# Kernel tuning notes

Measured on AMD Instinct MI355X. Metric: run time of the kernel, lower is better.

The kernel has to match this reference:

```python
import jax, jax.numpy as jnp
import numpy as np

DIM = 512
NUM_EXPERTS = 8
HID = 4 * DIM
B, S = 2, 2048


def setup_inputs() -> dict:
    key = jax.random.key(0)
    ks = jax.random.split(key, 7)
    sc = 0.02
    x = jax.random.normal(ks[0], (B, S, DIM), dtype=jnp.float32)
    Wr = jax.random.normal(ks[1], (DIM, NUM_EXPERTS), dtype=jnp.float32) * sc
    br = jnp.zeros((NUM_EXPERTS,), dtype=jnp.float32)
    W1 = jax.random.normal(ks[2], (NUM_EXPERTS, DIM, HID), dtype=jnp.float32) * sc
    b1 = jnp.zeros((NUM_EXPERTS, HID), dtype=jnp.float32)
    W2 = jax.random.normal(ks[3], (NUM_EXPERTS, HID, DIM), dtype=jnp.float32) * sc
    b2 = jnp.zeros((NUM_EXPERTS, DIM), dtype=jnp.float32)
    return {"x": x, "Wr": Wr, "br": br, "W1": W1, "b1": b1, "W2": W2, "b2": b2}


def reference(x, Wr, br, W1, b1, W2, b2):
    b, s, d = x.shape
    E = Wr.shape[1]
    xf = x.reshape(-1, d)                                   # [N, d]
    N = xf.shape[0]
    logits = xf @ Wr + br                                   # [N, E]
    probs = jax.nn.softmax(logits, axis=-1)
    top_w, top_idx = jax.lax.top_k(probs, 2)                # [N, 2]
    top_w = jax.nn.softmax(top_w, axis=-1)                  # renormalize top-2
    # combine weight per (token, expert); topk indices are distinct so add is safe
    comb = jnp.zeros((N, E), dtype=xf.dtype)
    comb = comb.at[jnp.arange(N)[:, None], top_idx].add(top_w)  # [N, E]
    # dense per-expert MLP (eval mode: dropout is identity); exact GELU as nn.GELU
    h = jax.nn.gelu(jnp.einsum('nd,edf->enf', xf, W1) + b1[:, None, :], approximate=False)
    y = jnp.einsum('enf,efd->end', h, W2) + b2[:, None, :]  # [E, N, d]
    out = jnp.einsum('end,ne->nd', y, comb)                 # weighted combine
    # load-balancing loss
    load = jnp.zeros((E,), dtype=jnp.float32).at[top_idx.reshape(-1)].add(1.0)
    load = load / load.sum()
    lb_loss = jnp.sum((load - 1.0 / E) ** 2)
    return out.reshape(b, s, d), lb_loss, load
```

## Files before the change

### kernel.cpp

```cpp
#include <hip/hip_runtime.h>
#include <hip/hip_bf16.h>

#define DIMD 512
#define NEXP 8
#define HIDN 2048
#define NTOK 4096
#define NASG 8192

typedef short bf16x8 __attribute__((ext_vector_type(8)));
typedef float f32x4 __attribute__((ext_vector_type(4)));

__device__ inline unsigned short f2bf(float f) {
  __hip_bfloat16 h = __float2bfloat16(f);
  return __builtin_bit_cast(unsigned short, h);
}

__device__ inline void gl16(const void* g, void* l) {
  __builtin_amdgcn_global_load_lds(
      (const __attribute__((address_space(1))) unsigned int*)g,
      (__attribute__((address_space(3))) unsigned int*)l, 16, 0, 0);
}

__global__ __launch_bounds__(256) void transpose_both_kernel(
    const float* __restrict__ W1, const float* __restrict__ W2,
    unsigned short* __restrict__ w1t, unsigned short* __restrict__ w2t) {
  __shared__ float tile[64][65];
  int z = blockIdx.z;
  int e = z & 7;
  const float* src; unsigned short* dst; int R, C, r0, c0;
  if (z < 8) { src = W1; dst = w1t; R = DIMD; C = HIDN; c0 = blockIdx.x * 64; r0 = blockIdx.y * 64; }
  else       { src = W2; dst = w2t; R = HIDN; C = DIMD; r0 = blockIdx.x * 64; c0 = blockIdx.y * 64; }
  const float* s = src + (size_t)e * R * C;
  unsigned short* d = dst + (size_t)e * R * C;
  for (int i = threadIdx.x; i < 4096; i += 256) {
    int r = i >> 6, c = i & 63;
    tile[r][c] = s[(size_t)(r0 + r) * C + (c0 + c)];
  }
  __syncthreads();
  for (int i = threadIdx.x; i < 2048; i += 256) {
    int c = i >> 5;
    int r = (i & 31) * 2;
    unsigned lo = f2bf(tile[r][c]);
    unsigned hi = f2bf(tile[r + 1][c]);
    *reinterpret_cast<unsigned*>(d + (size_t)(c0 + c) * R + (r0 + r)) = lo | (hi << 16);
  }
}

__global__ __launch_bounds__(256) void router_kernel(const float* __restrict__ x,
                                                     const float* __restrict__ Wr,
                                                     const float* __restrict__ br,
                                                     int* __restrict__ tidx,
                                                     float* __restrict__ tw,
                                                     unsigned short* __restrict__ xb) {
  int lane = threadIdx.x & 63;
  int n = blockIdx.x * 4 + (threadIdx.x >> 6);
  const float* xr = x + (size_t)n * DIMD;
  unsigned short* xbr = xb + (size_t)n * DIMD;
  float acc[NEXP];
#pragma unroll
  for (int e = 0; e < NEXP; ++e) acc[e] = 0.f;
#pragma unroll
  for (int it = 0; it < 2; ++it) {
    int d0 = it * 256 + lane * 4;
    float4 xv = *reinterpret_cast<const float4*>(xr + d0);
    unsigned p0 = (unsigned)f2bf(xv.x) | ((unsigned)f2bf(xv.y) << 16);
    unsigned p1 = (unsigned)f2bf(xv.z) | ((unsigned)f2bf(xv.w) << 16);
    *reinterpret_cast<uint2*>(xbr + d0) = make_uint2(p0, p1);
    const float* wr = Wr + (size_t)d0 * NEXP;
#pragma unroll
    for (int j = 0; j < 4; ++j) {
      float xj = (&xv.x)[j];
#pragma unroll
      for (int e = 0; e < NEXP; ++e) acc[e] += xj * wr[j * NEXP + e];
    }
  }
#pragma unroll
  for (int e = 0; e < NEXP; ++e) {
    float v = acc[e];
#pragma unroll
    for (int off = 32; off > 0; off >>= 1) v += __shfl_xor(v, off, 64);
    acc[e] = v + br[e];
  }
  if (lane == 0) {
    float m = acc[0];
    for (int e = 1; e < NEXP; ++e) m = fmaxf(m, acc[e]);
    float p[NEXP], s = 0.f;
    for (int e = 0; e < NEXP; ++e) { p[e] = expf(acc[e] - m); s += p[e]; }
    float inv = 1.f / s;
    for (int e = 0; e < NEXP; ++e) p[e] *= inv;
    int i0 = 0; float p0 = p[0];
    for (int e = 1; e < NEXP; ++e) if (p[e] > p0) { p0 = p[e]; i0 = e; }
    int i1 = (i0 == 0) ? 1 : 0; float p1 = p[i1];
    for (int e = 0; e < NEXP; ++e) if (e != i0 && p[e] > p1) { p1 = p[e]; i1 = e; }
    float t = expf(p1 - p0);
    float w0 = 1.f / (1.f + t);
    tidx[2 * n] = i0; tidx[2 * n + 1] = i1;
    tw[2 * n] = w0; tw[2 * n + 1] = t * w0;
  }
}

__global__ __launch_bounds__(1024) void route_pack_kernel(const int* __restrict__ tidx,
                                                          int* __restrict__ off,
                                                          int* __restrict__ list,
                                                          float* __restrict__ out_tail) {
  int tid = threadIdx.x;
  int wv = tid >> 6, lane = tid & 63;

  int ids[8];
#pragma unroll
  for (int j = 0; j < 8; ++j) ids[j] = tidx[tid * 8 + j];

  int c[NEXP];
#pragma unroll
  for (int e = 0; e < NEXP; ++e) c[e] = 0;
#pragma unroll
  for (int j = 0; j < 8; ++j)
#pragma unroll
    for (int e = 0; e < NEXP; ++e) c[e] += (ids[j] == e) ? 1 : 0;

  int inc[NEXP];
#pragma unroll
  for (int e = 0; e < NEXP; ++e) {
    int v = c[e];
#pragma unroll
    for (int d = 1; d < 64; d <<= 1) {
      int t = __shfl_up(v, d, 64);
      if (lane >= d) v += t;
    }
    inc[e] = v;
  }

  __shared__ int wtot[NEXP][16];
  __shared__ int wbase[NEXP][16];
  __shared__ int ebase[NEXP];
  if (lane == 63) {
#pragma unroll
    for (int e = 0; e < NEXP; ++e) wtot[e][wv] = inc[e];
  }
  __syncthreads();
  if (tid == 0) {
    int o = 0;
    float lb = 0.f;
    for (int e = 0; e < NEXP; ++e) {
      int s = 0;
      for (int w = 0; w < 16; ++w) { wbase[e][w] = s; s += wtot[e][w]; }
      ebase[e] = o;
      off[e] = o;
      o += s;
      float l = (float)s / (float)NASG;
      out_tail[1 + e] = l;
      float dd = l - 0.125f;
      lb += dd * dd;
    }
    off[NEXP] = o;
    out_tail[0] = lb;
  }
  __syncthreads();

  int pos[NEXP];
#pragma unroll
  for (int e = 0; e < NEXP; ++e)
    pos[e] = ebase[e] + wbase[e][wv] + (inc[e] - c[e]);

#pragma unroll
  for (int j = 0; j < 8; ++j) {
    int e = ids[j];
    int p = 0;
#pragma unroll
    for (int k = 0; k < NEXP; ++k)
      if (e == k) { p = pos[k]; pos[k] = p + 1; }
    list[p] = tid * 8 + j;
  }
}

__global__ __launch_bounds__(256) void gemm1_kernel(
    const unsigned short* __restrict__ xb,
    const unsigned short* __restrict__ w1t,
    const float* __restrict__ b1,
    const int* __restrict__ off,
    const int* __restrict__ list,
    unsigned short* __restrict__ H) {
  int e = blockIdx.z;
  int offe = off[e];
  int cnt_e = off[e + 1] - offe;
  int m0 = blockIdx.y * 128;
  if (m0 >= cnt_e) return;
  int n0 = blockIdx.x * 128;

  __shared__ char ldsb[65536];

  int tid = threadIdx.x, wv = tid >> 6, lane = tid & 63;
  int rsub = lane >> 3, sw = lane & 7;
  int ks = sw ^ rsub;

  const unsigned short* w1e = w1t + (size_t)e * HIDN * DIMD;
  const unsigned short* asrc[4];
  const unsigned short* bsrc[4];
#pragma unroll
  for (int i = 0; i < 4; ++i) {
    int r = wv * 32 + i * 8 + rsub;
    int rr = m0 + r;
    int tok = 0;
    if (rr < cnt_e) tok = list[offe + rr] >> 1;
    asrc[i] = xb + (size_t)tok * DIMD + ks * 8;
    bsrc[i] = w1e + (size_t)(n0 + r) * DIMD + ks * 8;
  }

  f32x4 zero = {0.f, 0.f, 0.f, 0.f};
  f32x4 acc[4][4];
#pragma unroll
  for (int m = 0; m < 4; ++m)
#pragma unroll
    for (int n = 0; n < 4; ++n) acc[m][n] = zero;

  int wave_m = wv >> 1, wave_n = wv & 1;
  int lane16 = lane & 15, kq = lane >> 4;
  int swzr = (lane16 & 7) << 4;

  const int T = DIMD / 64;
#pragma unroll
  for (int i = 0; i < 4; ++i) {
    gl16(asrc[i], ldsb + (wv * 32 + i * 8) * 128);
    gl16(bsrc[i], ldsb + 16384 + (wv * 32 + i * 8) * 128);
  }
  __syncthreads();

  for (int t = 0; t < T; ++t) {
    char* cb = ldsb + (t & 1) * 32768;
    if (t + 1 < T) {
      char* nb = ldsb + ((t + 1) & 1) * 32768;
      int k0 = (t + 1) * 64;
#pragma unroll
      for (int i = 0; i < 4; ++i) {
        gl16(asrc[i] + k0, nb + (wv * 32 + i * 8) * 128);
        gl16(bsrc[i] + k0, nb + 16384 + (wv * 32 + i * 8) * 128);
      }
    }
#pragma unroll
    for (int kk = 0; kk < 2; ++kk) {
      bf16x8 af[4], bfr[4];
#pragma unroll
      for (int m = 0; m < 4; ++m)
        af[m] = *reinterpret_cast<const bf16x8*>(
            cb + (((wave_m * 64 + m * 16 + lane16) * 128 + kk * 64 + kq * 16) ^ swzr));
#pragma unroll
      for (int n = 0; n < 4; ++n)
        bfr[n] = *reinterpret_cast<const bf16x8*>(
            cb + 16384 + (((wave_n * 64 + n * 16 + lane16) * 128 + kk * 64 + kq * 16) ^ swzr));
#pragma unroll
      for (int m = 0; m < 4; ++m)
#pragma unroll
        for (int n = 0; n < 4; ++n)
          acc[m][n] = __builtin_amdgcn_mfma_f32_16x16x32_bf16(af[m], bfr[n], acc[m][n], 0, 0, 0);
    }
    __syncthreads();
  }

  unsigned short* Ct = (unsigned short*)ldsb;
  const float* b1e = b1 + e * HIDN;
#pragma unroll
  for (int n = 0; n < 4; ++n) {
    int cl = wave_n * 64 + n * 16 + lane16;
    float bias = b1e[n0 + cl];
#pragma unroll
    for (int m = 0; m < 4; ++m) {
#pragma unroll
      for (int q = 0; q < 4; ++q) {
        int rl = wave_m * 64 + m * 16 + kq * 4 + q;
        float v = acc[m][n][q] + bias;
        float g = 0.5f * v * (1.f + erff(v * 0.70710678118654752f));
        Ct[rl * 136 + cl] = f2bf(g);
      }
    }
  }
  __syncthreads();
  for (int u = tid; u < 2048; u += 256) {
    int rl = u >> 4, c8 = (u & 15) * 8;
    int r = m0 + rl;
    if (r < cnt_e) {
      uint4 v = *reinterpret_cast<const uint4*>(Ct + rl * 136 + c8);
      *reinterpret_cast<uint4*>(H + (size_t)(offe + r) * HIDN + n0 + c8) = v;
    }
  }
}

__global__ __launch_bounds__(256) void gemm2_kernel(
    const unsigned short* __restrict__ H,
    const unsigned short* __restrict__ w2t,
    const float* __restrict__ b2,
    const int* __restrict__ off,
    const int* __restrict__ list,
    const float* __restrict__ tw,
    float* __restrict__ Yw) {
  int e = blockIdx.z;
  int offe = off[e];
  int cnt_e = off[e + 1] - offe;
  int m0 = blockIdx.y * 128;
  if (m0 >= cnt_e) return;
  int n0 = blockIdx.x * 128;

  __shared__ char ldsb[65536];

  int tid = threadIdx.x, wv = tid >> 6, lane = tid & 63;
  int rsub = lane >> 3, sw = lane & 7;
  int ks = sw ^ rsub;

  const unsigned short* w2e = w2t + (size_t)e * DIMD * HIDN;
  const unsigned short* asrc[4];
  const unsigned short* bsrc[4];
#pragma unroll
  for (int i = 0; i < 4; ++i) {
    int r = wv * 32 + i * 8 + rsub;
    int rowa = offe + m0 + r;
    if (rowa > NASG - 1) rowa = NASG - 1;
    asrc[i] = H + (size_t)rowa * HIDN + ks * 8;
    bsrc[i] = w2e + (size_t)(n0 + r) * HIDN + ks * 8;
  }

  f32x4 zero = {0.f, 0.f, 0.f, 0.f};
  f32x4 acc[4][4];
#pragma unroll
  for (int m = 0; m < 4; ++m)
#pragma unroll
    for (int n = 0; n < 4; ++n) acc[m][n] = zero;

  int wave_m = wv >> 1, wave_n = wv & 1;
  int lane16 = lane & 15, kq = lane >> 4;
  int swzr = (lane16 & 7) << 4;

  const int T = HIDN / 64;
#pragma unroll
  for (int i = 0; i < 4; ++i) {
    gl16(asrc[i], ldsb + (wv * 32 + i * 8) * 128);
    gl16(bsrc[i], ldsb + 16384 + (wv * 32 + i * 8) * 128);
  }
  __syncthreads();

  for (int t = 0; t < T; ++t) {
    char* cb = ldsb + (t & 1) * 32768;
    if (t + 1 < T) {
      char* nb = ldsb + ((t + 1) & 1) * 32768;
      int k0 = (t + 1) * 64;
#pragma unroll
      for (int i = 0; i < 4; ++i) {
        gl16(asrc[i] + k0, nb + (wv * 32 + i * 8) * 128);
        gl16(bsrc[i] + k0, nb + 16384 + (wv * 32 + i * 8) * 128);
      }
    }
#pragma unroll
    for (int kk = 0; kk < 2; ++kk) {
      bf16x8 af[4], bfr[4];
#pragma unroll
      for (int m = 0; m < 4; ++m)
        af[m] = *reinterpret_cast<const bf16x8*>(
            cb + (((wave_m * 64 + m * 16 + lane16) * 128 + kk * 64 + kq * 16) ^ swzr));
#pragma unroll
      for (int n = 0; n < 4; ++n)
        bfr[n] = *reinterpret_cast<const bf16x8*>(
            cb + 16384 + (((wave_n * 64 + n * 16 + lane16) * 128 + kk * 64 + kq * 16) ^ swzr));
#pragma unroll
      for (int m = 0; m < 4; ++m)
#pragma unroll
        for (int n = 0; n < 4; ++n)
          acc[m][n] = __builtin_amdgcn_mfma_f32_16x16x32_bf16(af[m], bfr[n], acc[m][n], 0, 0, 0);
    }
    __syncthreads();
  }

  const float* b2e = b2 + e * DIMD;
  float bias[4];
#pragma unroll
  for (int n = 0; n < 4; ++n) bias[n] = b2e[n0 + wave_n * 64 + n * 16 + lane16];
#pragma unroll
  for (int m = 0; m < 4; ++m) {
#pragma unroll
    for (int q = 0; q < 4; ++q) {
      int r = m0 + wave_m * 64 + m * 16 + kq * 4 + q;
      if (r < cnt_e) {
        int a = list[offe + r];
        float w = tw[a];
        float* yrow = Yw + (size_t)a * DIMD;
#pragma unroll
        for (int n = 0; n < 4; ++n) {
          int col = n0 + wave_n * 64 + n * 16 + lane16;
          yrow[col] = w * (acc[m][n][q] + bias[n]);
        }
      }
    }
  }
}

__global__ __launch_bounds__(256) void combine_kernel(const float* __restrict__ Yw,
                                                      float* __restrict__ out) {
  int i = (blockIdx.x * 256 + threadIdx.x) * 4;
  int n = i >> 9;
  int d = i & 511;
  float4 a = *reinterpret_cast<const float4*>(Yw + (size_t)(2 * n) * DIMD + d);
  float4 b = *reinterpret_cast<const float4*>(Yw + (size_t)(2 * n + 1) * DIMD + d);
  float4 o;
  o.x = a.x + b.x; o.y = a.y + b.y; o.z = a.z + b.z; o.w = a.w + b.w;
  *reinterpret_cast<float4*>(out + i) = o;
}

extern "C" void kernel_launch(void* const* d_in, const int* in_sizes, int n_in,
                              void* d_out, int out_size, void* d_ws, size_t ws_size,
                              hipStream_t stream) {
  const float* x  = (const float*)d_in[0];
  const float* Wr = (const float*)d_in[1];
  const float* br = (const float*)d_in[2];
  const float* W1 = (const float*)d_in[3];
  const float* b1 = (const float*)d_in[4];
  const float* W2 = (const float*)d_in[5];
  const float* b2 = (const float*)d_in[6];
  float* out = (float*)d_out;

  char* ws = (char*)d_ws;
  unsigned short* xb  = (unsigned short*)ws;  ws += (size_t)NTOK * DIMD * 2;
  unsigned short* w1t = (unsigned short*)ws;  ws += (size_t)NEXP * HIDN * DIMD * 2;
  unsigned short* w2t = (unsigned short*)ws;  ws += (size_t)NEXP * DIMD * HIDN * 2;
  unsigned short* H   = (unsigned short*)ws;  ws += (size_t)NASG * HIDN * 2;
  float* Yw = (float*)ws;                     ws += (size_t)NASG * DIMD * 4;
  float* tw = (float*)ws;                     ws += (size_t)NASG * 4;
  int* tidx = (int*)ws;                       ws += (size_t)NASG * 4;
  int* list = (int*)ws;                       ws += (size_t)NASG * 4;
  int* offp = (int*)ws;

  transpose_both_kernel<<<dim3(32, 8, 16), 256, 0, stream>>>(W1, W2, w1t, w2t);
  router_kernel<<<NTOK / 4, 256, 0, stream>>>(x, Wr, br, tidx, tw, xb);
  route_pack_kernel<<<1, 1024, 0, stream>>>(tidx, offp, list, out + (size_t)NTOK * DIMD);
  gemm1_kernel<<<dim3(HIDN / 128, NASG / 128, NEXP), 256, 0, stream>>>(xb, w1t, b1, offp, list, H);
  gemm2_kernel<<<dim3(DIMD / 128, NASG / 128, NEXP), 256, 0, stream>>>(H, w2t, b2, offp, list, tw, Yw);
  combine_kernel<<<2048, 256, 0, stream>>>(Yw, out);
}
```

Baseline: 124.7 us.

## Halve GEMM K-tile to 32 with packed-row swizzle and reorder grid dimensions

Both grouped expert GEMMs now stage 32-wide K slices instead of 64, with two rows packed per 128-byte LDS line under a new XOR swizzle. This halves LDS use per block (64KB to 32-36KB) so more blocks can be resident per CU. The grid is also reordered so the expert index varies fastest, which changes block scheduling order and likely spreads work across experts. The cost is twice as many K iterations and barriers per tile, with fewer MFMAs between syncs.

Measured after the change: 118.5 us. 4.9% less time.

```diff
diff --git a/kernel.cpp b/kernel.cpp
--- a/kernel.cpp
+++ b/kernel.cpp
@@ -173,6 +173,7 @@
   }
 }
 
+
 __global__ __launch_bounds__(256) void gemm1_kernel(
     const unsigned short* __restrict__ xb,
     const unsigned short* __restrict__ w1t,
@@ -180,31 +181,35 @@
     const int* __restrict__ off,
     const int* __restrict__ list,
     unsigned short* __restrict__ H) {
-  int e = blockIdx.z;
+  int e = blockIdx.x;
   int offe = off[e];
   int cnt_e = off[e + 1] - offe;
-  int m0 = blockIdx.y * 128;
+  int n0 = blockIdx.y * 128;
+  int m0 = blockIdx.z * 128;
   if (m0 >= cnt_e) return;
-  int n0 = blockIdx.x * 128;
-
-  __shared__ char ldsb[65536];
+
+  __shared__ char ldsb[36864];
 
   int tid = threadIdx.x, wv = tid >> 6, lane = tid & 63;
-  int rsub = lane >> 3, sw = lane & 7;
-  int ks = sw ^ rsub;
+  int rp = lane >> 3, sl = lane & 7;
+  int sx = sl ^ rp;
+  int rowadd = rp * 2 + (sx >> 2);
+  int kq = sx & 3;
 
   const unsigned short* w1e = w1t + (size_t)e * HIDN * DIMD;
-  const unsigned short* asrc[4];
-  const unsigned short* bsrc[4];
-#pragma unroll
-  for (int i = 0; i < 4; ++i) {
-    int r = wv * 32 + i * 8 + rsub;
+  const unsigned short* asrc[2];
+  const unsigned short* bsrc[2];
+#pragma unroll
+  for (int i = 0; i < 2; ++i) {
+    int r = wv * 32 + i * 16 + rowadd;
     int rr = m0 + r;
     int tok = 0;
     if (rr < cnt_e) tok = list[offe + rr] >> 1;
-    asrc[i] = xb + (size_t)tok * DIMD + ks * 8;
-    bsrc[i] = w1e + (size_t)(n0 + r) * DIMD + ks * 8;
-  }
+    asrc[i] = xb + (size_t)tok * DIMD + kq * 8;
+    bsrc[i] = w1e + (size_t)(n0 + r) * DIMD + kq * 8;
+  }
+  int dstA0 = wv * 2048;
+  int dstA1 = wv * 2048 + 1024;
 
   f32x4 zero = {0.f, 0.f, 0.f, 0.f};
   f32x4 acc[4][4];
@@ -214,45 +219,43 @@
     for (int n = 0; n < 4; ++n) acc[m][n] = zero;
 
   int wave_m = wv >> 1, wave_n = wv & 1;
-  int lane16 = lane & 15, kq = lane >> 4;
-  int swzr = (lane16 & 7) << 4;
-
-  const int T = DIMD / 64;
-#pragma unroll
-  for (int i = 0; i < 4; ++i) {
-    gl16(asrc[i], ldsb + (wv * 32 + i * 8) * 128);
-    gl16(bsrc[i], ldsb + 16384 + (wv * 32 + i * 8) * 128);
-  }
+  int lane16 = lane & 15, kq4 = lane >> 4;
+  int ra[4], rb[4];
+#pragma unroll
+  for (int m = 0; m < 4; ++m) {
+    int r = wave_m * 64 + m * 16 + lane16;
+    ra[m] = (r >> 1) * 128 + ((((kq4 + (r & 1) * 4)) ^ ((r >> 1) & 7)) << 4);
+    int rn = wave_n * 64 + m * 16 + lane16;
+    rb[m] = (rn >> 1) * 128 + ((((kq4 + (rn & 1) * 4)) ^ ((rn >> 1) & 7)) << 4);
+  }
+
+  const int T = DIMD / 32;
+  gl16(asrc[0], ldsb + dstA0);
+  gl16(asrc[1], ldsb + dstA1);
+  gl16(bsrc[0], ldsb + 8192 + dstA0);
+  gl16(bsrc[1], ldsb + 8192 + dstA1);
   __syncthreads();
 
   for (int t = 0; t < T; ++t) {
-    char* cb = ldsb + (t & 1) * 32768;
+    char* cb = ldsb + (t & 1) * 16384;
     if (t + 1 < T) {
-      char* nb = ldsb + ((t + 1) & 1) * 32768;
-      int k0 = (t + 1) * 64;
-#pragma unroll
-      for (int i = 0; i < 4; ++i) {
-        gl16(asrc[i] + k0, nb + (wv * 32 + i * 8) * 128);
-        gl16(bsrc[i] + k0, nb + 16384 + (wv * 32 + i * 8) * 128);
-      }
-    }
-#pragma unroll
-    for (int kk = 0; kk < 2; ++kk) {
-      bf16x8 af[4], bfr[4];
-#pragma unroll
-      for (int m = 0; m < 4; ++m)
-        af[m] = *reinterpret_cast<const bf16x8*>(
-            cb + (((wave_m * 64 + m * 16 + lane16) * 128 + kk * 64 + kq * 16) ^ swzr));
+      char* nb = ldsb + ((t + 1) & 1) * 16384;
+      int k0 = (t + 1) * 32;
+      gl16(asrc[0] + k0, nb + dstA0);
+      gl16(asrc[1] + k0, nb + dstA1);
+      gl16(bsrc[0] + k0, nb + 8192 + dstA0);
+      gl16(bsrc[1] + k0, nb + 8192 + dstA1);
+    }
+    bf16x8 af[4], bfr[4];
+#pragma unroll
+    for (int m = 0; m < 4; ++m) af[m] = *reinterpret_cast<const bf16x8*>(cb + ra[m]);
+#pragma unroll
+    for (int n = 0; n < 4; ++n) bfr[n] = *reinterpret_cast<const bf16x8*>(cb + 8192 + rb[n]);
+#pragma unroll
+    for (int m = 0; m < 4; ++m)
 #pragma unroll
       for (int n = 0; n < 4; ++n)
-        bfr[n] = *reinterpret_cast<const bf16x8*>(
-            cb + 16384 + (((wave_n * 64 + n * 16 + lane16) * 128 + kk * 64 + kq * 16) ^ swzr));
-#pragma unroll
-      for (int m = 0; m < 4; ++m)
-#pragma unroll
-        for (int n = 0; n < 4; ++n)
-          acc[m][n] = __builtin_amdgcn_mfma_f32_16x16x32_bf16(af[m], bfr[n], acc[m][n], 0, 0, 0);
-    }
+        acc[m][n] = __builtin_amdgcn_mfma_f32_16x16x32_bf16(af[m], bfr[n], acc[m][n], 0, 0, 0);
     __syncthreads();
   }
 
@@ -266,7 +269,7 @@
     for (int m = 0; m < 4; ++m) {
 #pragma unroll
       for (int q = 0; q < 4; ++q) {
-        int rl = wave_m * 64 + m * 16 + kq * 4 + q;
+        int rl = wave_m * 64 + m * 16 + kq4 * 4 + q;
         float v = acc[m][n][q] + bias;
         float g = 0.5f * v * (1.f + erff(v * 0.70710678118654752f));
         Ct[rl * 136 + cl] = f2bf(g);
@@ -292,30 +295,34 @@
     const int* __restrict__ list,
     const float* __restrict__ tw,
     float* __restrict__ Yw) {
-  int e = blockIdx.z;
+  int e = blockIdx.x;
   int offe = off[e];
   int cnt_e = off[e + 1] - offe;
-  int m0 = blockIdx.y * 128;
+  int n0 = blockIdx.y * 128;
+  int m0 = blockIdx.z * 128;
   if (m0 >= cnt_e) return;
-  int n0 = blockIdx.x * 128;
-
-  __shared__ char ldsb[65536];
+
+  __shared__ char ldsb[32768];
 
   int tid = threadIdx.x, wv = tid >> 6, lane = tid & 63;
-  int rsub = lane >> 3, sw = lane & 7;
-  int ks = sw ^ rsub;
+  int rp = lane >> 3, sl = lane & 7;
+  int sx = sl ^ rp;
+  int rowadd = rp * 2 + (sx >> 2);
+  int kq = sx & 3;
 
   const unsigned short* w2e = w2t + (size_t)e * DIMD * HIDN;
-  const unsigned short* asrc[4];
-  const unsigned short* bsrc[4];
-#pragma unroll
-  for (int i = 0; i < 4; ++i) {
-    int r = wv * 32 + i * 8 + rsub;
+  const unsigned short* asrc[2];
+  const unsigned short* bsrc[2];
+#pragma unroll
+  for (int i = 0; i < 2; ++i) {
+    int r = wv * 32 + i * 16 + rowadd;
     int rowa = offe + m0 + r;
     if (rowa > NASG - 1) rowa = NASG - 1;
-    asrc[i] = H + (size_t)rowa * HIDN + ks * 8;
-    bsrc[i] = w2e + (size_t)(n0 + r) * HIDN + ks * 8;
-  }
+    asrc[i] = H + (size_t)rowa * HIDN + kq * 8;
+    bsrc[i] = w2e + (size_t)(n0 + r) * HIDN + kq * 8;
+  }
+  int dstA0 = wv * 2048;
+  int dstA1 = wv * 2048 + 1024;
 
   f32x4 zero = {0.f, 0.f, 0.f, 0.f};
   f32x4 acc[4][4];
@@ -325,45 +332,43 @@
     for (int n = 0; n < 4; ++n) acc[m][n] = zero;
 
   int wave_m = wv >> 1, wave_n = wv & 1;
-  int lane16 = lane & 15, kq = lane >> 4;
-  int swzr = (lane16 & 7) << 4;
-
-  const int T = HIDN / 64;
-#pragma unroll
-  for (int i = 0; i < 4; ++i) {
-    gl16(asrc[i], ldsb + (wv * 32 + i * 8) * 128);
-    gl16(bsrc[i], ldsb + 16384 + (wv * 32 + i * 8) * 128);
-  }
+  int lane16 = lane & 15, kq4 = lane >> 4;
+  int ra[4], rb[4];
+#pragma unroll
+  for (int m = 0; m < 4; ++m) {
+    int r = wave_m * 64 + m * 16 + lane16;
+    ra[m] = (r >> 1) * 128 + ((((kq4 + (r & 1) * 4)) ^ ((r >> 1) & 7)) << 4);
+    int rn = wave_n * 64 + m * 16 + lane16;
+    rb[m] = (rn >> 1) * 128 + ((((kq4 + (rn & 1) * 4)) ^ ((rn >> 1) & 7)) << 4);
+  }
+
+  const int T = HIDN / 32;
+  gl16(asrc[0], ldsb + dstA0);
+  gl16(asrc[1], ldsb + dstA1);
+  gl16(bsrc[0], ldsb + 8192 + dstA0);
+  gl16(bsrc[1], ldsb + 8192 + dstA1);
   __syncthreads();
 
   for (int t = 0; t < T; ++t) {
-    char* cb = ldsb + (t & 1) * 32768;
+    char* cb = ldsb + (t & 1) * 16384;
     if (t + 1 < T) {
-      char* nb = ldsb + ((t + 1) & 1) * 32768;
-      int k0 = (t + 1) * 64;
-#pragma unroll
-      for (int i = 0; i < 4; ++i) {
-        gl16(asrc[i] + k0, nb + (wv * 32 + i * 8) * 128);
-        gl16(bsrc[i] + k0, nb + 16384 + (wv * 32 + i * 8) * 128);
-      }
-    }
-#pragma unroll
-    for (int kk = 0; kk < 2; ++kk) {
-      bf16x8 af[4], bfr[4];
-#pragma unroll
-      for (int m = 0; m < 4; ++m)
-        af[m] = *reinterpret_cast<const bf16x8*>(
-            cb + (((wave_m * 64 + m * 16 + lane16) * 128 + kk * 64 + kq * 16) ^ swzr));
+      char* nb = ldsb + ((t + 1) & 1) * 16384;
+      int k0 = (t + 1) * 32;
+      gl16(asrc[0] + k0, nb + dstA0);
+      gl16(asrc[1] + k0, nb + dstA1);
+      gl16(bsrc[0] + k0, nb + 8192 + dstA0);
+      gl16(bsrc[1] + k0, nb + 8192 + dstA1);
+    }
+    bf16x8 af[4], bfr[4];
+#pragma unroll
+    for (int m = 0; m < 4; ++m) af[m] = *reinterpret_cast<const bf16x8*>(cb + ra[m]);
+#pragma unroll
+    for (int n = 0; n < 4; ++n) bfr[n] = *reinterpret_cast<const bf16x8*>(cb + 8192 + rb[n]);
+#pragma unroll
+    for (int m = 0; m < 4; ++m)
 #pragma unroll
       for (int n = 0; n < 4; ++n)
-        bfr[n] = *reinterpret_cast<const bf16x8*>(
-            cb + 16384 + (((wave_n * 64 + n * 16 + lane16) * 128 + kk * 64 + kq * 16) ^ swzr));
-#pragma unroll
-      for (int m = 0; m < 4; ++m)
-#pragma unroll
-        for (int n = 0; n < 4; ++n)
-          acc[m][n] = __builtin_amdgcn_mfma_f32_16x16x32_bf16(af[m], bfr[n], acc[m][n], 0, 0, 0);
-    }
+        acc[m][n] = __builtin_amdgcn_mfma_f32_16x16x32_bf16(af[m], bfr[n], acc[m][n], 0, 0, 0);
     __syncthreads();
   }
 
@@ -375,7 +380,7 @@
   for (int m = 0; m < 4; ++m) {
 #pragma unroll
     for (int q = 0; q < 4; ++q) {
-      int r = m0 + wave_m * 64 + m * 16 + kq * 4 + q;
+      int r = m0 + wave_m * 64 + m * 16 + kq4 * 4 + q;
       if (r < cnt_e) {
         int a = list[offe + r];
         float w = tw[a];
@@ -428,7 +433,7 @@
   transpose_both_kernel<<<dim3(32, 8, 16), 256, 0, stream>>>(W1, W2, w1t, w2t);
   router_kernel<<<NTOK / 4, 256, 0, stream>>>(x, Wr, br, tidx, tw, xb);
   route_pack_kernel<<<1, 1024, 0, stream>>>(tidx, offp, list, out + (size_t)NTOK * DIMD);
-  gemm1_kernel<<<dim3(HIDN / 128, NASG / 128, NEXP), 256, 0, stream>>>(xb, w1t, b1, offp, list, H);
-  gemm2_kernel<<<dim3(DIMD / 128, NASG / 128, NEXP), 256, 0, stream>>>(H, w2t, b2, offp, list, tw, Yw);
+  gemm1_kernel<<<dim3(NEXP, HIDN / 128, NASG / 128), 256, 0, stream>>>(xb, w1t, b1, offp, list, H);
+  gemm2_kernel<<<dim3(NEXP, DIMD / 128, NASG / 128), 256, 0, stream>>>(H, w2t, b2, offp, list, tw, Yw);
   combine_kernel<<<2048, 256, 0, stream>>>(Yw, out);
 }
```
